# Optimization experiments

Measured on AMD Instinct MI355X. Metric: run time of the kernel, lower is better.

## Reference

```python
import jax, jax.numpy as jnp
import numpy as np

HEAD_SIZE = 64
NUM_HEADS = 16
D_MODEL = HEAD_SIZE * NUM_HEADS  # 1024
B, S = 2, 2048


def setup_inputs() -> dict:
    key = jax.random.key(0)
    ks = jax.random.split(key, 13)
    sc = 1.0 / np.sqrt(D_MODEL)
    inp = {
        'queries': jax.random.normal(ks[0], (B, S, D_MODEL), jnp.float32),
        'keys': jax.random.normal(ks[1], (B, S, D_MODEL), jnp.float32),
        'values': jax.random.normal(ks[2], (B, S, D_MODEL), jnp.float32),
        'mask': jax.random.randint(ks[3], (B, NUM_HEADS, S, S), 0, 2, jnp.int32),
        # nn.Linear weights (out,in) and biases
        'Wq': jax.random.normal(ks[4], (D_MODEL, D_MODEL), jnp.float32) * sc,
        'bq': jax.random.normal(ks[5], (D_MODEL,), jnp.float32) * sc,
        'Wk': jax.random.normal(ks[6], (D_MODEL, D_MODEL), jnp.float32) * sc,
        'bk': jax.random.normal(ks[7], (D_MODEL,), jnp.float32) * sc,
        'Wv': jax.random.normal(ks[8], (D_MODEL, D_MODEL), jnp.float32) * sc,
        'bv': jax.random.normal(ks[9], (D_MODEL,), jnp.float32) * sc,
        'Wy': jax.random.normal(ks[10], (D_MODEL, D_MODEL), jnp.float32) * sc,
        'by': jax.random.normal(ks[11], (D_MODEL,), jnp.float32) * sc,
        # extra nn.Parameter biases (initialized to zeros in the module)
        'bq2': jnp.zeros((D_MODEL,), jnp.float32),
        'bk2': jnp.zeros((D_MODEL,), jnp.float32),
        'bv2': jnp.zeros((D_MODEL,), jnp.float32),
        'by2': jnp.zeros((D_MODEL,), jnp.float32),
    }
    return inp


def _split_heads(x):
    b, s, _ = x.shape
    return x.reshape(b, s, NUM_HEADS, HEAD_SIZE).transpose(0, 2, 1, 3)  # [B,H,S,D]


def _merge_heads(x):
    b, h, s, d = x.shape
    return x.transpose(0, 2, 1, 3).reshape(b, s, h * d)


def mha(queries, keys, values, mask, Wq, bq, bq2, Wk, bk, bk2, Wv, bv, bv2, Wy, by, by2):
    q = queries @ Wq.T + bq + bq2
    k = keys @ Wk.T + bk + bk2
    v = values @ Wv.T + bv + bv2
    q, k, v = _split_heads(q), _split_heads(k), _split_heads(v)  # [B,H,S,D]
    scores = jnp.einsum('bhqd,bhkd->bhqk', q, k) / np.sqrt(HEAD_SIZE).astype(np.float32)
    m = mask.astype(scores.dtype)
    scores = scores * m - 1e4 * (1.0 - m)
    w = jax.nn.softmax(scores, axis=-1)
    out = jnp.einsum('bhqk,bhkd->bhqd', w, v)
    y = _merge_heads(out)  # [B,S,H*D]
    return y @ Wy.T + by + by2


def reference(queries, keys, values, mask, Wq, bq, Wk, bk, Wv, bv, Wy, by, bq2, bk2, bv2, by2):
    return mha(queries, keys, values, mask, Wq, bq, bq2, Wk, bk, bk2, Wv, bv, bv2, Wy, by, by2)
```

## Files before the change

### kernel.cpp

```cpp
#include <hip/hip_runtime.h>
#include <math.h>


typedef _Float16 h8 __attribute__((ext_vector_type(8)));
typedef _Float16 h4 __attribute__((ext_vector_type(4)));
typedef float f4 __attribute__((ext_vector_type(4)));

#define S_LEN 2048
#define DM 1024
#define NH 16
#define HD 64

__global__ __launch_bounds__(256, 2) void qkv_proj_kernel(
    const float* __restrict__ Xq, const float* __restrict__ Xk, const float* __restrict__ Xv,
    const float* __restrict__ Wq, const float* __restrict__ Wk, const float* __restrict__ Wv,
    const float* __restrict__ bq, const float* __restrict__ bk, const float* __restrict__ bv,
    const float* __restrict__ bq2, const float* __restrict__ bk2, const float* __restrict__ bv2,
    _Float16* __restrict__ oq, _Float16* __restrict__ okk, _Float16* __restrict__ ov)
{
    const int z = blockIdx.z;
    const float* X  = (z == 0) ? Xq  : (z == 1) ? Xk  : Xv;
    const float* W  = (z == 0) ? Wq  : (z == 1) ? Wk  : Wv;
    const float* b1 = (z == 0) ? bq  : (z == 1) ? bk  : bv;
    const float* b2 = (z == 0) ? bq2 : (z == 1) ? bk2 : bv2;
    _Float16* outp  = (z == 0) ? oq  : (z == 1) ? okk : ov;

    __shared__ _Float16 As[128][56];
    __shared__ _Float16 Bs[128][56];

    const int tid  = threadIdx.x;
    const int lane = tid & 63;
    const int wave = tid >> 6;
    const int l16  = lane & 15;
    const int g    = lane >> 4;
    const int wm   = (wave >> 1) * 64;
    const int wn   = (wave & 1) * 64;
    const int m0   = blockIdx.x * 128;
    const int n0   = blockIdx.y * 128;

    f4 acc[4][4] = {};

    for (int k0 = 0; k0 < 1024; k0 += 32) {
        __syncthreads();
        #pragma unroll
        for (int r = 0; r < 4; ++r) {
            int f = tid + 256 * r;
            int row = f >> 3;
            int c4  = (f & 7) * 4;
            f4 xa = *(const f4*)(X + (size_t)(m0 + row) * 1024 + k0 + c4);
            f4 xb = *(const f4*)(W + (size_t)(n0 + row) * 1024 + k0 + c4);
            As[row][c4 + 0] = (_Float16)xa.x; As[row][c4 + 1] = (_Float16)xa.y;
            As[row][c4 + 2] = (_Float16)xa.z; As[row][c4 + 3] = (_Float16)xa.w;
            Bs[row][c4 + 0] = (_Float16)xb.x; Bs[row][c4 + 1] = (_Float16)xb.y;
            Bs[row][c4 + 2] = (_Float16)xb.z; Bs[row][c4 + 3] = (_Float16)xb.w;
        }
        __syncthreads();

        h8 af[4], bf[4];
        #pragma unroll
        for (int i = 0; i < 4; ++i) af[i] = *(const h8*)&As[wm + i * 16 + l16][g * 8];
        #pragma unroll
        for (int j = 0; j < 4; ++j) bf[j] = *(const h8*)&Bs[wn + j * 16 + l16][g * 8];
        #pragma unroll
        for (int i = 0; i < 4; ++i)
            #pragma unroll
            for (int j = 0; j < 4; ++j)
                acc[i][j] = __builtin_amdgcn_mfma_f32_16x16x32_f16(af[i], bf[j], acc[i][j], 0, 0, 0);
    }

    #pragma unroll
    for (int i = 0; i < 4; ++i)
        #pragma unroll
        for (int j = 0; j < 4; ++j)
            #pragma unroll
            for (int r = 0; r < 4; ++r) {
                int gm = m0 + wm + i * 16 + g * 4 + r;
                int gn = n0 + wn + j * 16 + l16;
                float val = acc[i][j][r] + b1[gn] + b2[gn];
                int b = gm >> 11, s = gm & 2047;
                int h = gn >> 6,  d = gn & 63;
                outp[(((size_t)(b * NH + h) * S_LEN + s) << 6) + d] = (_Float16)val;
            }
}

__global__ __launch_bounds__(256) void transpose_v_kernel(
    const _Float16* __restrict__ v, _Float16* __restrict__ vt)
{
    const int bh = blockIdx.x;
    const int s0 = blockIdx.y * 64;
    __shared__ _Float16 t[64][65];
    const int tid = threadIdx.x;

    #pragma unroll
    for (int r = 0; r < 2; ++r) {
        int u = tid + 256 * r;
        int row = u >> 3, c8 = (u & 7) * 8;
        h8 hv = *(const h8*)(v + ((size_t)bh * S_LEN + s0 + row) * 64 + c8);
        #pragma unroll
        for (int e = 0; e < 8; ++e) t[row][c8 + e] = hv[e];
    }
    __syncthreads();
    #pragma unroll
    for (int r = 0; r < 2; ++r) {
        int u = tid + 256 * r;
        int d = u >> 3, p8 = (u & 7) * 8;
        h8 hv;
        #pragma unroll
        for (int e = 0; e < 8; ++e) {
            int p = p8 + e;
            int c = (p & 3) * 16 + (p >> 2);
            hv[e] = t[c][d];
        }
        *(h8*)(vt + ((size_t)bh * 64 + d) * S_LEN + s0 + p8) = hv;
    }
}

__global__ __launch_bounds__(256) void pack_mask_kernel(
    const int* __restrict__ mask, unsigned long long* __restrict__ pm)
{
    const int lane = threadIdx.x & 63;
    const size_t wid0   = (size_t)blockIdx.x * 4 + (threadIdx.x >> 6);
    const size_t nwaves = (size_t)gridDim.x * 4;
    const size_t nwords = (size_t)32 * S_LEN * 32;
    for (size_t w = wid0; w < nwords; w += nwaves) {
        int mv = mask[(w << 6) | lane];
        unsigned long long b = __ballot(mv != 0);
        if (lane == 0) pm[w] = b;
    }
}

__global__ __launch_bounds__(256, 3) void attn_kernel(
    const _Float16* __restrict__ q_ws, const _Float16* __restrict__ k_ws,
    const _Float16* __restrict__ vt_ws, const unsigned long long* __restrict__ pm,
    _Float16* __restrict__ o_ws)
{
    const int tid  = threadIdx.x;
    const int lane = tid & 63;
    const int wave = tid >> 6;
    const int g    = lane >> 4;
    const int l16  = lane & 15;
    const int qt   = blockIdx.x;
    const int bh   = blockIdx.y;
    const int q0   = qt * 128;

    __shared__ _Float16 Ks[64][72];
    __shared__ _Float16 Vs[64][72];
    __shared__ _Float16 Ps[128][72];

    h8 qf[2][2];
    #pragma unroll
    for (int i = 0; i < 2; ++i)
        #pragma unroll
        for (int ks = 0; ks < 2; ++ks)
            qf[i][ks] = *(const h8*)(q_ws +
                ((size_t)bh * S_LEN + q0 + wave * 32 + i * 16 + l16) * 64 + ks * 32 + g * 8);

    f4 oacc[2][4] = {};
    float lsum[2][4] = {};

    const unsigned long long* pmrow =
        pm + ((size_t)bh * S_LEN + q0 + wave * 32) * 32;

    for (int kt = 0; kt < 32; ++kt) {
        const int k0 = kt * 64;

        unsigned long long mw[2][4];
        #pragma unroll
        for (int i = 0; i < 2; ++i)
            #pragma unroll
            for (int r = 0; r < 4; ++r)
                mw[i][r] = pmrow[(size_t)(i * 16 + g * 4 + r) * 32 + kt];

        __syncthreads();
        #pragma unroll
        for (int r = 0; r < 2; ++r) {
            int u = tid + 256 * r;
            int row = u >> 3, c8 = (u & 7) * 8;
            *(h8*)&Ks[row][c8] = *(const h8*)(k_ws + ((size_t)bh * S_LEN + k0 + row) * 64 + c8);
            *(h8*)&Vs[row][c8] = *(const h8*)(vt_ws + ((size_t)bh * 64 + row) * S_LEN + k0 + c8);
        }
        __syncthreads();

        f4 sacc[2][4] = {};
        #pragma unroll
        for (int ks = 0; ks < 2; ++ks) {
            h8 kf[4];
            #pragma unroll
            for (int j = 0; j < 4; ++j) kf[j] = *(const h8*)&Ks[j * 16 + l16][ks * 32 + g * 8];
            #pragma unroll
            for (int i = 0; i < 2; ++i)
                #pragma unroll
                for (int j = 0; j < 4; ++j)
                    sacc[i][j] = __builtin_amdgcn_mfma_f32_16x16x32_f16(qf[i][ks], kf[j], sacc[i][j], 0, 0, 0);
        }

        #pragma unroll
        for (int i = 0; i < 2; ++i)
            #pragma unroll
            for (int r = 0; r < 4; ++r) {
                unsigned long long w = mw[i][r] >> l16;
                unsigned lo = (unsigned)w, hi = (unsigned)(w >> 32);
                float p0 = (lo & 1u)         ? __expf(fmaf(sacc[i][0][r], 0.125f, -5.0f)) : 0.0f;
                float p1 = ((lo >> 16) & 1u) ? __expf(fmaf(sacc[i][1][r], 0.125f, -5.0f)) : 0.0f;
                float p2 = (hi & 1u)         ? __expf(fmaf(sacc[i][2][r], 0.125f, -5.0f)) : 0.0f;
                float p3 = ((hi >> 16) & 1u) ? __expf(fmaf(sacc[i][3][r], 0.125f, -5.0f)) : 0.0f;
                lsum[i][r] += (p0 + p1) + (p2 + p3);
                h4 ph = { (_Float16)p0, (_Float16)p1, (_Float16)p2, (_Float16)p3 };
                *(h4*)&Ps[wave * 32 + i * 16 + g * 4 + r][l16 * 4] = ph;
            }

        #pragma unroll
        for (int ks = 0; ks < 2; ++ks) {
            h8 pf[2], vf[4];
            #pragma unroll
            for (int i = 0; i < 2; ++i)  pf[i]  = *(const h8*)&Ps[wave * 32 + i * 16 + l16][ks * 32 + g * 8];
            #pragma unroll
            for (int jd = 0; jd < 4; ++jd) vf[jd] = *(const h8*)&Vs[jd * 16 + l16][ks * 32 + g * 8];
            #pragma unroll
            for (int i = 0; i < 2; ++i)
                #pragma unroll
                for (int jd = 0; jd < 4; ++jd)
                    oacc[i][jd] = __builtin_amdgcn_mfma_f32_16x16x32_f16(pf[i], vf[jd], oacc[i][jd], 0, 0, 0);
        }
    }

    const int b = bh >> 4, h = bh & 15;
    #pragma unroll
    for (int i = 0; i < 2; ++i)
        #pragma unroll
        for (int r = 0; r < 4; ++r) {
            float l = lsum[i][r];
            l += __shfl_xor(l, 1);
            l += __shfl_xor(l, 2);
            l += __shfl_xor(l, 4);
            l += __shfl_xor(l, 8);
            float inv = 1.0f / l;
            int row = q0 + wave * 32 + i * 16 + g * 4 + r;
            #pragma unroll
            for (int jd = 0; jd < 4; ++jd) {
                int d = jd * 16 + l16;
                o_ws[((size_t)b * S_LEN + row) * DM + h * 64 + d] = (_Float16)(oacc[i][jd][r] * inv);
            }
        }
}

__global__ __launch_bounds__(256, 2) void out_proj_kernel(
    const _Float16* __restrict__ A, const float* __restrict__ W,
    const float* __restrict__ b1, const float* __restrict__ b2,
    float* __restrict__ out)
{
    __shared__ _Float16 As[128][56];
    __shared__ _Float16 Bs[128][56];

    const int tid  = threadIdx.x;
    const int lane = tid & 63;
    const int wave = tid >> 6;
    const int l16  = lane & 15;
    const int g    = lane >> 4;
    const int wm   = (wave >> 1) * 64;
    const int wn   = (wave & 1) * 64;
    const int m0   = blockIdx.x * 128;
    const int n0   = blockIdx.y * 128;

    f4 acc[4][4] = {};

    for (int k0 = 0; k0 < 1024; k0 += 32) {
        __syncthreads();
        #pragma unroll
        for (int r = 0; r < 2; ++r) {
            int u = tid + 256 * r;
            int row = u >> 2, c8 = (u & 3) * 8;
            *(h8*)&As[row][c8] = *(const h8*)(A + (size_t)(m0 + row) * 1024 + k0 + c8);
        }
        #pragma unroll
        for (int r = 0; r < 4; ++r) {
            int f = tid + 256 * r;
            int row = f >> 3, c4 = (f & 7) * 4;
            f4 xb = *(const f4*)(W + (size_t)(n0 + row) * 1024 + k0 + c4);
            Bs[row][c4 + 0] = (_Float16)xb.x; Bs[row][c4 + 1] = (_Float16)xb.y;
            Bs[row][c4 + 2] = (_Float16)xb.z; Bs[row][c4 + 3] = (_Float16)xb.w;
        }
        __syncthreads();

        h8 af[4], bf[4];
        #pragma unroll
        for (int i = 0; i < 4; ++i) af[i] = *(const h8*)&As[wm + i * 16 + l16][g * 8];
        #pragma unroll
        for (int j = 0; j < 4; ++j) bf[j] = *(const h8*)&Bs[wn + j * 16 + l16][g * 8];
        #pragma unroll
        for (int i = 0; i < 4; ++i)
            #pragma unroll
            for (int j = 0; j < 4; ++j)
                acc[i][j] = __builtin_amdgcn_mfma_f32_16x16x32_f16(af[i], bf[j], acc[i][j], 0, 0, 0);
    }

    #pragma unroll
    for (int i = 0; i < 4; ++i)
        #pragma unroll
        for (int j = 0; j < 4; ++j)
            #pragma unroll
            for (int r = 0; r < 4; ++r) {
                int gm = m0 + wm + i * 16 + g * 4 + r;
                int gn = n0 + wn + j * 16 + l16;
                out[(size_t)gm * 1024 + gn] = acc[i][j][r] + b1[gn] + b2[gn];
            }
}

extern "C" void kernel_launch(void* const* d_in, const int* in_sizes, int n_in,
                              void* d_out, int out_size, void* d_ws, size_t ws_size,
                              hipStream_t stream)
{
    (void)in_sizes; (void)n_in; (void)out_size; (void)ws_size;
    const float* queries = (const float*)d_in[0];
    const float* keys    = (const float*)d_in[1];
    const float* values  = (const float*)d_in[2];
    const int*   mask    = (const int*)d_in[3];
    const float* Wq  = (const float*)d_in[4];
    const float* bq  = (const float*)d_in[5];
    const float* Wk  = (const float*)d_in[6];
    const float* bk  = (const float*)d_in[7];
    const float* Wv  = (const float*)d_in[8];
    const float* bv  = (const float*)d_in[9];
    const float* Wy  = (const float*)d_in[10];
    const float* by  = (const float*)d_in[11];
    const float* bq2 = (const float*)d_in[12];
    const float* bk2 = (const float*)d_in[13];
    const float* bv2 = (const float*)d_in[14];
    const float* by2 = (const float*)d_in[15];
    float* out = (float*)d_out;

    char* ws = (char*)d_ws;
    const size_t MB8 = (size_t)8 * 1024 * 1024;
    _Float16* q_ws  = (_Float16*)(ws);
    _Float16* k_ws  = (_Float16*)(ws + 1 * MB8);
    _Float16* v_ws  = (_Float16*)(ws + 2 * MB8);
    _Float16* vt_ws = (_Float16*)(ws + 3 * MB8);
    _Float16* o_ws  = (_Float16*)(ws + 4 * MB8);
    unsigned long long* pm = (unsigned long long*)(ws + 5 * MB8);

    qkv_proj_kernel<<<dim3(32, 8, 3), 256, 0, stream>>>(
        queries, keys, values, Wq, Wk, Wv, bq, bk, bv, bq2, bk2, bv2,
        q_ws, k_ws, v_ws);
    transpose_v_kernel<<<dim3(32, 32), 256, 0, stream>>>(v_ws, vt_ws);
    pack_mask_kernel<<<2048, 256, 0, stream>>>(mask, pm);
    attn_kernel<<<dim3(16, 32), 256, 0, stream>>>(q_ws, k_ws, vt_ws, pm, o_ws);
    out_proj_kernel<<<dim3(32, 8), 256, 0, stream>>>(o_ws, Wy, by, by2, out);
}
```

Measured before the change: 958.5 us.

## Fuse mask packing into attention kernel with register-prefetched int mask tiles

Removes the separate pack_mask kernel and its bitmask round-trip through memory. The attention kernel now reads the int32 mask directly, prefetching the next key tile's mask into registers while the current one is packed into per-wave shared-memory nibbles. The per-element mask bits are then read back from LDS during the softmax step. In exchange it uses more registers (occupancy hint lowered from 3 to 2 blocks), adds shared memory, and issues 128 MB of strided int mask loads inside the attention loop.

```diff
diff --git a/kernel.cpp b/kernel.cpp
--- a/kernel.cpp
+++ b/kernel.cpp
@@ -115,23 +115,9 @@
     }
 }
 
-__global__ __launch_bounds__(256) void pack_mask_kernel(
-    const int* __restrict__ mask, unsigned long long* __restrict__ pm)
-{
-    const int lane = threadIdx.x & 63;
-    const size_t wid0   = (size_t)blockIdx.x * 4 + (threadIdx.x >> 6);
-    const size_t nwaves = (size_t)gridDim.x * 4;
-    const size_t nwords = (size_t)32 * S_LEN * 32;
-    for (size_t w = wid0; w < nwords; w += nwaves) {
-        int mv = mask[(w << 6) | lane];
-        unsigned long long b = __ballot(mv != 0);
-        if (lane == 0) pm[w] = b;
-    }
-}
-
-__global__ __launch_bounds__(256, 3) void attn_kernel(
+__global__ __launch_bounds__(256, 2) void attn_kernel(
     const _Float16* __restrict__ q_ws, const _Float16* __restrict__ k_ws,
-    const _Float16* __restrict__ vt_ws, const unsigned long long* __restrict__ pm,
+    const _Float16* __restrict__ vt_ws, const int* __restrict__ mask,
     _Float16* __restrict__ o_ws)
 {
     const int tid  = threadIdx.x;
@@ -146,6 +132,7 @@
     __shared__ _Float16 Ks[64][72];
     __shared__ _Float16 Vs[64][72];
     __shared__ _Float16 Ps[128][72];
+    __shared__ unsigned int Ms[4][128];
 
     h8 qf[2][2];
     #pragma unroll
@@ -158,18 +145,20 @@
     f4 oacc[2][4] = {};
     float lsum[2][4] = {};
 
-    const unsigned long long* pmrow =
-        pm + ((size_t)bh * S_LEN + q0 + wave * 32) * 32;
+    const int* mbase = mask + ((size_t)bh * S_LEN + q0 + wave * 32) * S_LEN;
+    const int mrow = lane >> 4;
+
+    int4 mv[8];
+    #pragma unroll
+    for (int c = 0; c < 8; ++c) {
+        int chunk = 64 * c + lane;
+        mv[c] = *(const int4*)(mbase + (size_t)(chunk >> 4) * S_LEN + (chunk & 15) * 4);
+    }
+    (void)mrow;
 
     for (int kt = 0; kt < 32; ++kt) {
         const int k0 = kt * 64;
-
-        unsigned long long mw[2][4];
-        #pragma unroll
-        for (int i = 0; i < 2; ++i)
-            #pragma unroll
-            for (int r = 0; r < 4; ++r)
-                mw[i][r] = pmrow[(size_t)(i * 16 + g * 4 + r) * 32 + kt];
+        const int kn = ((kt + 1) & 31) * 64;
 
         __syncthreads();
         #pragma unroll
@@ -195,15 +184,33 @@
         }
 
         #pragma unroll
+        for (int c = 0; c < 8; ++c) {
+            int chunk = 64 * c + lane;
+            unsigned nib = (unsigned)(mv[c].x != 0)
+                         | ((unsigned)(mv[c].y != 0) << 1)
+                         | ((unsigned)(mv[c].z != 0) << 2)
+                         | ((unsigned)(mv[c].w != 0) << 3);
+            int rr = chunk >> 4, c4 = chunk & 15;
+            ((unsigned char*)&Ms[wave][0])[rr * 16 + (c4 & 3) * 4 + (c4 >> 2)] =
+                (unsigned char)nib;
+        }
+        #pragma unroll
+        for (int c = 0; c < 8; ++c) {
+            int chunk = 64 * c + lane;
+            mv[c] = *(const int4*)(mbase + (size_t)(chunk >> 4) * S_LEN + kn + (chunk & 15) * 4);
+        }
+
+        #pragma unroll
         for (int i = 0; i < 2; ++i)
             #pragma unroll
             for (int r = 0; r < 4; ++r) {
-                unsigned long long w = mw[i][r] >> l16;
-                unsigned lo = (unsigned)w, hi = (unsigned)(w >> 32);
-                float p0 = (lo & 1u)         ? __expf(fmaf(sacc[i][0][r], 0.125f, -5.0f)) : 0.0f;
-                float p1 = ((lo >> 16) & 1u) ? __expf(fmaf(sacc[i][1][r], 0.125f, -5.0f)) : 0.0f;
-                float p2 = (hi & 1u)         ? __expf(fmaf(sacc[i][2][r], 0.125f, -5.0f)) : 0.0f;
-                float p3 = ((hi >> 16) & 1u) ? __expf(fmaf(sacc[i][3][r], 0.125f, -5.0f)) : 0.0f;
+                int row_local = i * 16 + g * 4 + r;
+                unsigned word = Ms[wave][row_local * 4 + (l16 >> 2)];
+                unsigned sh = l16 & 3;
+                float p0 = ((word >> (sh))      & 1u) ? __expf(fmaf(sacc[i][0][r], 0.125f, -5.0f)) : 0.0f;
+                float p1 = ((word >> (8 + sh))  & 1u) ? __expf(fmaf(sacc[i][1][r], 0.125f, -5.0f)) : 0.0f;
+                float p2 = ((word >> (16 + sh)) & 1u) ? __expf(fmaf(sacc[i][2][r], 0.125f, -5.0f)) : 0.0f;
+                float p3 = ((word >> (24 + sh)) & 1u) ? __expf(fmaf(sacc[i][3][r], 0.125f, -5.0f)) : 0.0f;
                 lsum[i][r] += (p0 + p1) + (p2 + p3);
                 h4 ph = { (_Float16)p0, (_Float16)p1, (_Float16)p2, (_Float16)p3 };
                 *(h4*)&Ps[wave * 32 + i * 16 + g * 4 + r][l16 * 4] = ph;
@@ -336,13 +343,11 @@
     _Float16* v_ws  = (_Float16*)(ws + 2 * MB8);
     _Float16* vt_ws = (_Float16*)(ws + 3 * MB8);
     _Float16* o_ws  = (_Float16*)(ws + 4 * MB8);
-    unsigned long long* pm = (unsigned long long*)(ws + 5 * MB8);
 
     qkv_proj_kernel<<<dim3(32, 8, 3), 256, 0, stream>>>(
         queries, keys, values, Wq, Wk, Wv, bq, bk, bv, bq2, bk2, bv2,
         q_ws, k_ws, v_ws);
     transpose_v_kernel<<<dim3(32, 32), 256, 0, stream>>>(v_ws, vt_ws);
-    pack_mask_kernel<<<2048, 256, 0, stream>>>(mask, pm);
-    attn_kernel<<<dim3(16, 32), 256, 0, stream>>>(q_ws, k_ws, vt_ws, pm, o_ws);
+    attn_kernel<<<dim3(16, 32), 256, 0, stream>>>(q_ws, k_ws, vt_ws, mask, o_ws);
     out_proj_kernel<<<dim3(32, 8), 256, 0, stream>>>(o_ws, Wy, by, by2, out);
 }
```

New measurement: 876.6 us. -8.5%, faster.

## Fuse mask packing into QKV GEMM and split attention keys across two halves

Applied to the files above, without the earlier changes.

Mask packing now runs inside the QKV projection kernel: each wave issues nontemporal loads of mask words while staging its tiles and ballots them after the tile sync, so the separate pack kernel goes away and its memory traffic overlaps with GEMM compute. The attention kernel is split into two key halves, doubling the grid to improve occupancy. Each half writes unnormalized fp32 partial outputs and row sums, which the output projection combines and normalizes while loading its A tile. This relies on the mask being fixed (no max subtraction), and it adds fp32 partial-output traffic and extra register pressure in the QKV kernel.

```diff
diff --git a/kernel.cpp b/kernel.cpp
--- a/kernel.cpp
+++ b/kernel.cpp
@@ -10,12 +10,14 @@
 #define DM 1024
 #define NH 16
 #define HD 64
+#define NWORDS 2097152
 
 __global__ __launch_bounds__(256, 2) void qkv_proj_kernel(
     const float* __restrict__ Xq, const float* __restrict__ Xk, const float* __restrict__ Xv,
     const float* __restrict__ Wq, const float* __restrict__ Wk, const float* __restrict__ Wv,
     const float* __restrict__ bq, const float* __restrict__ bk, const float* __restrict__ bv,
     const float* __restrict__ bq2, const float* __restrict__ bk2, const float* __restrict__ bv2,
+    const int* __restrict__ mask, unsigned long long* __restrict__ pm,
     _Float16* __restrict__ oq, _Float16* __restrict__ okk, _Float16* __restrict__ ov)
 {
     const int z = blockIdx.z;
@@ -38,9 +40,23 @@
     const int m0   = blockIdx.x * 128;
     const int n0   = blockIdx.y * 128;
 
+    const int bidf  = blockIdx.x + 32 * (blockIdx.y + 8 * blockIdx.z);
+    const int wslot = bidf * 4 + wave;
+
     f4 acc[4][4] = {};
 
-    for (int k0 = 0; k0 < 1024; k0 += 32) {
+    for (int ki = 0; ki < 32; ++ki) {
+        const int k0 = ki * 32;
+
+        int mloc[22];
+        const size_t wbase = ((size_t)wslot * 32 + ki) * 22;
+        #pragma unroll
+        for (int t = 0; t < 22; ++t) {
+            size_t w = wbase + t;
+            mloc[t] = (w < NWORDS)
+                ? __builtin_nontemporal_load(mask + ((w << 6) | (size_t)lane)) : 0;
+        }
+
         __syncthreads();
         #pragma unroll
         for (int r = 0; r < 4; ++r) {
@@ -49,12 +65,19 @@
             int c4  = (f & 7) * 4;
             f4 xa = *(const f4*)(X + (size_t)(m0 + row) * 1024 + k0 + c4);
             f4 xb = *(const f4*)(W + (size_t)(n0 + row) * 1024 + k0 + c4);
-            As[row][c4 + 0] = (_Float16)xa.x; As[row][c4 + 1] = (_Float16)xa.y;
-            As[row][c4 + 2] = (_Float16)xa.z; As[row][c4 + 3] = (_Float16)xa.w;
-            Bs[row][c4 + 0] = (_Float16)xb.x; Bs[row][c4 + 1] = (_Float16)xb.y;
-            Bs[row][c4 + 2] = (_Float16)xb.z; Bs[row][c4 + 3] = (_Float16)xb.w;
-        }
-        __syncthreads();
+            h4 ha = { (_Float16)xa.x, (_Float16)xa.y, (_Float16)xa.z, (_Float16)xa.w };
+            h4 hb = { (_Float16)xb.x, (_Float16)xb.y, (_Float16)xb.z, (_Float16)xb.w };
+            *(h4*)&As[row][c4] = ha;
+            *(h4*)&Bs[row][c4] = hb;
+        }
+        __syncthreads();
+
+        #pragma unroll
+        for (int t = 0; t < 22; ++t) {
+            unsigned long long bl = __ballot(mloc[t] != 0);
+            size_t w = wbase + t;
+            if (lane == 0 && w < NWORDS) pm[w] = bl;
+        }
 
         h8 af[4], bf[4];
         #pragma unroll
@@ -115,24 +138,10 @@
     }
 }
 
-__global__ __launch_bounds__(256) void pack_mask_kernel(
-    const int* __restrict__ mask, unsigned long long* __restrict__ pm)
-{
-    const int lane = threadIdx.x & 63;
-    const size_t wid0   = (size_t)blockIdx.x * 4 + (threadIdx.x >> 6);
-    const size_t nwaves = (size_t)gridDim.x * 4;
-    const size_t nwords = (size_t)32 * S_LEN * 32;
-    for (size_t w = wid0; w < nwords; w += nwaves) {
-        int mv = mask[(w << 6) | lane];
-        unsigned long long b = __ballot(mv != 0);
-        if (lane == 0) pm[w] = b;
-    }
-}
-
-__global__ __launch_bounds__(256, 3) void attn_kernel(
+__global__ __launch_bounds__(256, 4) void attn_kernel(
     const _Float16* __restrict__ q_ws, const _Float16* __restrict__ k_ws,
     const _Float16* __restrict__ vt_ws, const unsigned long long* __restrict__ pm,
-    _Float16* __restrict__ o_ws)
+    float* __restrict__ o_part, float* __restrict__ l_ws)
 {
     const int tid  = threadIdx.x;
     const int lane = tid & 63;
@@ -141,6 +150,7 @@
     const int l16  = lane & 15;
     const int qt   = blockIdx.x;
     const int bh   = blockIdx.y;
+    const int half = blockIdx.z;
     const int q0   = qt * 128;
 
     __shared__ _Float16 Ks[64][72];
@@ -161,7 +171,7 @@
     const unsigned long long* pmrow =
         pm + ((size_t)bh * S_LEN + q0 + wave * 32) * 32;
 
-    for (int kt = 0; kt < 32; ++kt) {
+    for (int kt = half * 16; kt < half * 16 + 16; ++kt) {
         const int k0 = kt * 64;
 
         unsigned long long mw[2][4];
@@ -225,6 +235,7 @@
     }
 
     const int b = bh >> 4, h = bh & 15;
+    float* Op = o_part + (size_t)half * ((size_t)2 * S_LEN * DM);
     #pragma unroll
     for (int i = 0; i < 2; ++i)
         #pragma unroll
@@ -234,23 +245,24 @@
             l += __shfl_xor(l, 2);
             l += __shfl_xor(l, 4);
             l += __shfl_xor(l, 8);
-            float inv = 1.0f / l;
             int row = q0 + wave * 32 + i * 16 + g * 4 + r;
-            #pragma unroll
-            for (int jd = 0; jd < 4; ++jd) {
-                int d = jd * 16 + l16;
-                o_ws[((size_t)b * S_LEN + row) * DM + h * 64 + d] = (_Float16)(oacc[i][jd][r] * inv);
-            }
+            if (l16 == 0)
+                l_ws[(size_t)half * (32 * S_LEN) + (size_t)bh * S_LEN + row] = l;
+            #pragma unroll
+            for (int jd = 0; jd < 4; ++jd)
+                Op[((size_t)b * S_LEN + row) * DM + h * 64 + jd * 16 + l16] = oacc[i][jd][r];
         }
 }
 
 __global__ __launch_bounds__(256, 2) void out_proj_kernel(
-    const _Float16* __restrict__ A, const float* __restrict__ W,
-    const float* __restrict__ b1, const float* __restrict__ b2,
-    float* __restrict__ out)
+    const float* __restrict__ O1, const float* __restrict__ O2,
+    const float* __restrict__ l_ws,
+    const float* __restrict__ W, const float* __restrict__ b1,
+    const float* __restrict__ b2, float* __restrict__ out)
 {
     __shared__ _Float16 As[128][56];
     __shared__ _Float16 Bs[128][56];
+    __shared__ float invl[128][17];
 
     const int tid  = threadIdx.x;
     const int lane = tid & 63;
@@ -262,23 +274,44 @@
     const int m0   = blockIdx.x * 128;
     const int n0   = blockIdx.y * 128;
 
+    for (int u = tid; u < 2048; u += 256) {
+        int row = u >> 4, h = u & 15;
+        int gm = m0 + row;
+        int b = gm >> 11, s = gm & 2047;
+        size_t idx = (size_t)(b * NH + h) * S_LEN + s;
+        float l = l_ws[idx] + l_ws[(size_t)32 * S_LEN + idx];
+        invl[row][h] = 1.0f / l;
+    }
+
     f4 acc[4][4] = {};
 
     for (int k0 = 0; k0 < 1024; k0 += 32) {
+        const int h = k0 >> 6;
         __syncthreads();
         #pragma unroll
         for (int r = 0; r < 2; ++r) {
             int u = tid + 256 * r;
             int row = u >> 2, c8 = (u & 3) * 8;
-            *(h8*)&As[row][c8] = *(const h8*)(A + (size_t)(m0 + row) * 1024 + k0 + c8);
+            size_t base = (size_t)(m0 + row) * 1024 + k0 + c8;
+            f4 a0 = *(const f4*)(O1 + base);
+            f4 a1 = *(const f4*)(O1 + base + 4);
+            f4 c0 = *(const f4*)(O2 + base);
+            f4 c1 = *(const f4*)(O2 + base + 4);
+            float sc = invl[row][h];
+            h8 av;
+            av[0] = (_Float16)((a0.x + c0.x) * sc); av[1] = (_Float16)((a0.y + c0.y) * sc);
+            av[2] = (_Float16)((a0.z + c0.z) * sc); av[3] = (_Float16)((a0.w + c0.w) * sc);
+            av[4] = (_Float16)((a1.x + c1.x) * sc); av[5] = (_Float16)((a1.y + c1.y) * sc);
+            av[6] = (_Float16)((a1.z + c1.z) * sc); av[7] = (_Float16)((a1.w + c1.w) * sc);
+            *(h8*)&As[row][c8] = av;
         }
         #pragma unroll
         for (int r = 0; r < 4; ++r) {
             int f = tid + 256 * r;
             int row = f >> 3, c4 = (f & 7) * 4;
             f4 xb = *(const f4*)(W + (size_t)(n0 + row) * 1024 + k0 + c4);
-            Bs[row][c4 + 0] = (_Float16)xb.x; Bs[row][c4 + 1] = (_Float16)xb.y;
-            Bs[row][c4 + 2] = (_Float16)xb.z; Bs[row][c4 + 3] = (_Float16)xb.w;
+            h4 hb = { (_Float16)xb.x, (_Float16)xb.y, (_Float16)xb.z, (_Float16)xb.w };
+            *(h4*)&Bs[row][c4] = hb;
         }
         __syncthreads();
 
@@ -330,19 +363,20 @@
     float* out = (float*)d_out;
 
     char* ws = (char*)d_ws;
-    const size_t MB8 = (size_t)8 * 1024 * 1024;
+    const size_t MB = (size_t)1024 * 1024;
     _Float16* q_ws  = (_Float16*)(ws);
-    _Float16* k_ws  = (_Float16*)(ws + 1 * MB8);
-    _Float16* v_ws  = (_Float16*)(ws + 2 * MB8);
-    _Float16* vt_ws = (_Float16*)(ws + 3 * MB8);
-    _Float16* o_ws  = (_Float16*)(ws + 4 * MB8);
-    unsigned long long* pm = (unsigned long long*)(ws + 5 * MB8);
+    _Float16* k_ws  = (_Float16*)(ws +  8 * MB);
+    _Float16* v_ws  = (_Float16*)(ws + 16 * MB);
+    _Float16* vt_ws = (_Float16*)(ws + 24 * MB);
+    float*    o_pt  = (float*)   (ws + 32 * MB);
+    float*    l_ws  = (float*)   (ws + 64 * MB);
+    unsigned long long* pm = (unsigned long long*)(ws + 65 * MB);
 
     qkv_proj_kernel<<<dim3(32, 8, 3), 256, 0, stream>>>(
         queries, keys, values, Wq, Wk, Wv, bq, bk, bv, bq2, bk2, bv2,
-        q_ws, k_ws, v_ws);
+        mask, pm, q_ws, k_ws, v_ws);
     transpose_v_kernel<<<dim3(32, 32), 256, 0, stream>>>(v_ws, vt_ws);
-    pack_mask_kernel<<<2048, 256, 0, stream>>>(mask, pm);
-    attn_kernel<<<dim3(16, 32), 256, 0, stream>>>(q_ws, k_ws, vt_ws, pm, o_ws);
-    out_proj_kernel<<<dim3(32, 8), 256, 0, stream>>>(o_ws, Wy, by, by2, out);
-}
+    attn_kernel<<<dim3(16, 32, 2), 256, 0, stream>>>(q_ws, k_ws, vt_ws, pm, o_pt, l_ws);
+    out_proj_kernel<<<dim3(32, 8), 256, 0, stream>>>(o_pt, o_pt + (size_t)2 * S_LEN * DM,
+                                                     l_ws, Wy, by, by2, out);
+}
```

New measurement: 1.162 ms. +21.2%, slower.
